# Kernel optimization log

Measured on AMD Instinct MI355X. Metric: run time of the kernel, lower is better.

The kernel has to match this reference:

```python
import jax, jax.numpy as jnp
import numpy as np

N = 10000      # nodes
E = 160000     # edges (before self-loops)
F_IN = 128     # num_features
H1, D1 = 4, 256   # conv1: 4 heads x 256, concat -> 1024
D2 = 256          # conv2: 1 head x 256
NEG_SLOPE = 0.2


def setup_inputs() -> dict:
    key = jax.random.key(0)
    ks = jax.random.split(key, 12)
    def p(k, shape, fan):
        return jax.random.normal(k, shape, jnp.float32) / np.float32(np.sqrt(fan))
    return {
        "x": jax.random.normal(ks[0], (N, F_IN), jnp.float32),
        "edge_index": jax.random.randint(ks[1], (2, E), 0, N, jnp.int32),
        "W1": p(ks[2], (F_IN, H1 * D1), F_IN),
        "att_src1": p(ks[3], (H1, D1), D1),
        "att_dst1": p(ks[4], (H1, D1), D1),
        "b1": jnp.zeros((H1 * D1,), jnp.float32),
        "lin1_W": p(ks[5], (F_IN, H1 * D1), F_IN),
        "lin1_b": jnp.zeros((H1 * D1,), jnp.float32),
        "W2": p(ks[6], (H1 * D1, D2), H1 * D1),
        "att_src2": p(ks[7], (1, D2), D2),
        "att_dst2": p(ks[8], (1, D2), D2),
        "b2": jnp.zeros((D2,), jnp.float32),
        "lin2_W": p(ks[9], (H1 * D1, D2), H1 * D1),
        "lin2_b": jnp.zeros((D2,), jnp.float32),
    }


def gat_layer(x, src, dst, W, a_src, a_dst, b, heads, d):
    """PyG-style GATConv: transform, edgewise LeakyReLU attention,
    segment-softmax over destination neighborhoods, scatter-add, concat heads."""
    n = x.shape[0]
    h = (x @ W).reshape(n, heads, d)                       # [N, H, D]
    s_src = jnp.einsum('nhd,hd->nh', h, a_src)             # per-node scores
    s_dst = jnp.einsum('nhd,hd->nh', h, a_dst)
    e = jax.nn.leaky_relu(s_src[src] + s_dst[dst], NEG_SLOPE)   # [E, H]
    m = jax.ops.segment_max(e, dst, num_segments=n)        # stable softmax per dst
    p = jnp.exp(e - m[dst])
    z = jax.ops.segment_sum(p, dst, num_segments=n)
    alpha = p / (z[dst] + 1e-16)                           # [E, H]
    msg = h[src] * alpha[:, :, None]                       # [E, H, D]
    out = jax.ops.segment_sum(msg, dst, num_segments=n)    # [N, H, D]
    return out.reshape(n, heads * d) + b, alpha


def reference(x, edge_index, W1, att_src1, att_dst1, b1, lin1_W, lin1_b,
              W2, att_src2, att_dst2, b2, lin2_W, lin2_b):
    n = x.shape[0]
    loop = jnp.arange(n, dtype=edge_index.dtype)           # add self-loops (PyG default)
    src = jnp.concatenate([edge_index[0], loop])
    dst = jnp.concatenate([edge_index[1], loop])
    h1, alpha1 = gat_layer(x, src, dst, W1, att_src1, att_dst1, b1, H1, D1)
    h1 = jax.nn.elu(h1 + x @ lin1_W + lin1_b)              # conv1 + lin1 residual, ELU
    h2, _ = gat_layer(h1, src, dst, W2, att_src2, att_dst2, b2, 1, D2)
    out = h2 + h1 @ lin2_W + lin2_b                        # conv2 + lin2 residual
    return out, alpha1
```

## Files before the change

kernel.cpp:

```cpp
#include <hip/hip_runtime.h>
#include <hip/hip_bf16.h>
#include <math.h>

#define NN   10000
#define EE   160000
#define ETOT 170000
#define FIN  128
#define C1   1024
#define NH1  4
#define D1   256
#define D2   256
#define MAXD 96

typedef __attribute__((ext_vector_type(8))) short bf16x8;
typedef __attribute__((ext_vector_type(4))) float f32x4;

__device__ __forceinline__ float b2f(unsigned short u)
{
    union { unsigned int i; float f; } c; c.i = (unsigned int)u << 16; return c.f;
}
__device__ __forceinline__ unsigned short f2b(float x)
{
    return __builtin_bit_cast(unsigned short, __float2bfloat16(x));
}
__device__ __forceinline__ void split1(float x, unsigned short &h, unsigned short &l)
{
    __hip_bfloat16 hb = __float2bfloat16(x);
    float r = x - __bfloat162float(hb);
    h = __builtin_bit_cast(unsigned short, hb);
    l = __builtin_bit_cast(unsigned short, __float2bfloat16(r));
}

__device__ __forceinline__ void split_A_body(const float* __restrict__ X,
                                             unsigned short* __restrict__ A2,
                                             int M, int K, int idx)
{
    int kq4 = K >> 2;
    if (idx >= M * kq4) return;
    int m = idx / kq4, kq = idx % kq4;
    float4 v = *(const float4*)&X[(size_t)m * K + kq * 4];
    ushort4 h, l;
    split1(v.x, h.x, l.x); split1(v.y, h.y, l.y);
    split1(v.z, h.z, l.z); split1(v.w, h.w, l.w);
    unsigned short* row = A2 + (size_t)m * (2 * K);
    *(ushort4*)&row[kq * 4]     = h;
    *(ushort4*)&row[K + kq * 4] = l;
}

__device__ __forceinline__ void split_Bt_body(const float* __restrict__ B0,
                                              const float* __restrict__ B1,
                                              int K, int N0, int Ntot,
                                              unsigned short* __restrict__ Bt, int idx)
{
    int total = Ntot * (K >> 2);
    if (idx >= total) return;
    int n = idx % Ntot;
    int kq = idx / Ntot;
    int k = kq * 4;
    const float* B; int nc, nb;
    if (n < N0) { B = B0; nc = n; nb = N0; }
    else        { B = B1; nc = n - N0; nb = Ntot - N0; }
    float v0 = B[(size_t)(k + 0) * nb + nc];
    float v1 = B[(size_t)(k + 1) * nb + nc];
    float v2 = B[(size_t)(k + 2) * nb + nc];
    float v3 = B[(size_t)(k + 3) * nb + nc];
    ushort4 h, l;
    split1(v0, h.x, l.x); split1(v1, h.y, l.y);
    split1(v2, h.z, l.z); split1(v3, h.w, l.w);
    unsigned short* row = Bt + (size_t)n * (3 * K);
    *(ushort4*)&row[k]         = h;
    *(ushort4*)&row[K + k]     = h;
    *(ushort4*)&row[2 * K + k] = l;
}

__device__ __forceinline__ void split_Bt1_body(const float* __restrict__ W1,
                                               const float* __restrict__ lin1W,
                                               unsigned short* __restrict__ Bt, int idx)
{
    if (idx >= 1024 * 64) return;
    int n = idx & 1023;
    int k = (idx >> 10) * 4;
    float v[4];
    #pragma unroll
    for (int i = 0; i < 4; ++i) {
        int kk = k + i;
        v[i] = (kk < 128) ? W1[(size_t)kk * C1 + n] : lin1W[(size_t)(kk - 128) * C1 + n];
    }
    ushort4 h, l;
    split1(v[0], h.x, l.x); split1(v[1], h.y, l.y);
    split1(v[2], h.z, l.z); split1(v[3], h.w, l.w);
    unsigned short* row = Bt + (size_t)n * 768;
    *(ushort4*)&row[k]       = h;
    *(ushort4*)&row[256 + k] = h;
    *(ushort4*)&row[512 + k] = l;
}

__global__ __launch_bounds__(256)
void prep(const float* __restrict__ x, unsigned short* __restrict__ A1stk,
          const float* __restrict__ W1, const float* __restrict__ lin1_W,
          unsigned short* __restrict__ Bt1,
          const float* __restrict__ W2, const float* __restrict__ lin2_W,
          unsigned short* __restrict__ Bt2,
          const int* __restrict__ dstp, int* __restrict__ cnt,
          const float* __restrict__ as1, const float* __restrict__ ad1,
          float* __restrict__ w1s, float* __restrict__ w1d,
          const float* __restrict__ as2, const float* __restrict__ ad2,
          float* __restrict__ v2s, float* __restrict__ v2d)
{
    const int b = blockIdx.x, t = threadIdx.x;
    const int w = t >> 6, lane = t & 63;
    if (b < 1250) {
        split_A_body(x, A1stk, NN, FIN, b * 256 + t);
    } else if (b < 1506) {
        split_Bt1_body(W1, lin1_W, Bt1, (b - 1250) * 256 + t);
    } else if (b < 2018) {
        split_Bt_body(W2, lin2_W, C1, D2, 512, Bt2, (b - 1506) * 256 + t);
    } else if (b < 2683) {
        int e = (b - 2018) * 256 + t;
        if (e < ETOT) {
            int d = (e < EE) ? dstp[e] : (e - EE);
            atomicAdd(&cnt[d], 1);
        }
    } else if (b < 2939) {
        int gw = (b - 2683) * 4 + w;
        int k = gw >> 3, rem = gw & 7, h = rem >> 1, issd = rem & 1;
        const float* a = issd ? ad1 : as1;
        float4 wv = *(const float4*)&W1[(size_t)k * C1 + h * 256 + lane * 4];
        float4 av = *(const float4*)&a[h * 256 + lane * 4];
        float s = wv.x * av.x + wv.y * av.y + wv.z * av.z + wv.w * av.w;
        #pragma unroll
        for (int off = 32; off; off >>= 1) s += __shfl_xor(s, off);
        if (lane == 0) (issd ? w1d : w1s)[k * 4 + h] = s;
    } else {
        int gw = (b - 2939) * 4 + w;
        int k = gw >> 1, issd = gw & 1;
        const float* a = issd ? ad2 : as2;
        float4 wv = *(const float4*)&W2[(size_t)k * D2 + lane * 4];
        float4 av = *(const float4*)&a[lane * 4];
        float s = wv.x * av.x + wv.y * av.y + wv.z * av.z + wv.w * av.w;
        #pragma unroll
        for (int off = 32; off; off >>= 1) s += __shfl_xor(s, off);
        if (lane == 0) (issd ? v2d : v2s)[k] = s;
    }
}

__device__ __forceinline__ void glds16(const void* g, void* l)
{
    __builtin_amdgcn_global_load_lds((const __attribute__((address_space(1))) void*)g,
                                     (__attribute__((address_space(3))) void*)l, 16, 0, 0);
}

__global__ __launch_bounds__(256)
void gemm_l1(const unsigned short* __restrict__ Apx,
             const unsigned short* __restrict__ Ax,
             const unsigned short* __restrict__ Bt,
             unsigned short* __restrict__ h1split,
             int M, const float* __restrict__ bias0, const float* __restrict__ bias1)
{
    constexpr int BM = 128, BN = 128, BK = 32;
    constexpr int FJ = 4, FI = 4;
    constexpr int SLOTS = 4, SMASK = 3, SWSH = 1;
    constexpr int RPC = 16, ACH = 8, CPW = 4;
    constexpr int ABUF = BM * BK, BBUF = BN * BK;
    __shared__ __align__(16) unsigned short sA[2 * ABUF];
    __shared__ __align__(16) unsigned short sB[2 * BBUF];
    const int tid = threadIdx.x, w = tid >> 6, lane = tid & 63;
    const int cpx = gridDim.x >> 3;
    const int t0 = (blockIdx.x & 7) * cpx + (blockIdx.x >> 3);
    const int m0 = (t0 >> 3) * BM;
    const int n0 = (t0 & 7) * BN;
    const int hsel = n0 >> 8;
    const int wm = w >> 1, wn = w & 1;
    f32x4 acc[FI][FJ] = {};

    const unsigned short *gx[CPW], *gpx[CPW], *gb[CPW];
    int lofs[CPW]; bool isa[CPW];
    {
        const int r = lane / SLOTS, sl = lane % SLOTS;
        const int ssl = sl ^ ((r >> SWSH) & SMASK);
        #pragma unroll
        for (int cc = 0; cc < CPW; ++cc) {
            int c = w * CPW + cc;
            if (c < ACH) {
                int gm = m0 + c * RPC + r; if (gm >= M) gm = M - 1;
                gx[cc]  = Ax  + (size_t)gm * 256 + ssl * 8;
                gpx[cc] = Apx + (size_t)gm * 1024 + hsel * 256 + ssl * 8;
                gb[cc]  = nullptr;
                lofs[cc] = c * 512;
                isa[cc] = true;
            } else {
                int gn = n0 + (c - ACH) * RPC + r;
                gx[cc] = gpx[cc] = nullptr;
                gb[cc] = Bt + (size_t)gn * 768 + ssl * 8;
                lofs[cc] = (c - ACH) * 512;
                isa[cc] = false;
            }
        }
    }

    const int rAl = wm * 64 + (lane & 15);
    const int rBl = wn * 64 + (lane & 15);
    const int sIdx = lane >> 4;
    const int nit = 768 / BK;
    int cur = 0;

    auto stage = [&](int kk, int buf) {
        int rr = kk >> 7;
        bool px = !(rr & 1);
        int off = px ? ((rr == 2) ? 128 : 0) : ((rr == 3) ? 128 : 0);
        int kin = kk & 127;
        #pragma unroll
        for (int cc = 0; cc < CPW; ++cc) {
            if (isa[cc]) glds16((px ? gpx[cc] : gx[cc]) + off + kin, sA + buf * ABUF + lofs[cc]);
            else         glds16(gb[cc] + kk,                         sB + buf * BBUF + lofs[cc]);
        }
    };

    stage(0, 0);
    __syncthreads();
    for (int it = 0; it < nit; ++it) {
        if (it + 1 < nit) stage((it + 1) * BK, cur ^ 1);
        const unsigned short* cA = sA + cur * ABUF;
        const unsigned short* cB = sB + cur * BBUF;
        bf16x8 av[FJ], bv[FI];
        #pragma unroll
        for (int f = 0; f < FI; ++f) {
            int row = rBl + f * 16;
            bv[f] = *(const bf16x8*)&cB[row * BK + ((sIdx ^ ((row >> SWSH) & SMASK)) << 3)];
        }
        #pragma unroll
        for (int f = 0; f < FJ; ++f) {
            int row = rAl + f * 16;
            av[f] = *(const bf16x8*)&cA[row * BK + ((sIdx ^ ((row >> SWSH) & SMASK)) << 3)];
        }
        #pragma unroll
        for (int fj = 0; fj < FJ; ++fj)
            #pragma unroll
            for (int fi = 0; fi < FI; ++fi)
                acc[fi][fj] = __builtin_amdgcn_mfma_f32_16x16x32_bf16(
                    bv[fi], av[fj], acc[fi][fj], 0, 0, 0);
        __syncthreads();
        cur ^= 1;
    }

    const int lrow = lane & 15;
    const int lcol = (lane >> 4) << 2;
    #pragma unroll
    for (int fj = 0; fj < FJ; ++fj) {
        int row = m0 + wm * 64 + fj * 16 + lrow;
        if (row >= M) continue;
        #pragma unroll
        for (int fi = 0; fi < FI; ++fi) {
            int col = n0 + wn * 64 + fi * 16 + lcol;
            f32x4 v = acc[fi][fj];
            const float4 g0 = *(const float4*)&bias0[col];
            const float4 g1 = *(const float4*)&bias1[col];
            v[0] += g0.x + g1.x; v[1] += g0.y + g1.y;
            v[2] += g0.z + g1.z; v[3] += g0.w + g1.w;
            #pragma unroll
            for (int i = 0; i < 4; ++i) v[i] = v[i] > 0.f ? v[i] : expm1f(v[i]);
            ushort4 hi, lo;
            split1(v[0], hi.x, lo.x); split1(v[1], hi.y, lo.y);
            split1(v[2], hi.z, lo.z); split1(v[3], hi.w, lo.w);
            unsigned short* orow = h1split + (size_t)row * 2048;
            *(ushort4*)&orow[col]        = hi;
            *(ushort4*)&orow[C1 + col]   = lo;
        }
    }
}

template<int BN, int WM, int WN, int BK>
__global__ __launch_bounds__(256)
void gemm_split(const unsigned short* __restrict__ A, int lda, int ka2,
                const unsigned short* __restrict__ Bt, int keff,
                unsigned short* __restrict__ outPb, float* __restrict__ outR,
                int M, int nsplit, int ldR, int ntn,
                const float* __restrict__ bias0, const float* __restrict__ bias1)
{
    constexpr int BM   = 128;
    constexpr int WTM  = BM / WM,  WTN = BN / WN;
    constexpr int FJ   = WTM / 16, FI  = WTN / 16;
    constexpr int KS   = BK / 32;
    constexpr int SLOTS = BK / 8;
    constexpr int SMASK = SLOTS - 1;
    constexpr int SWSH  = (BK == 32) ? 1 : 0;
    constexpr int RPC  = 512 / BK;
    constexpr int ACH  = BM / RPC;
    constexpr int NCH  = (BM + BN) / RPC;
    constexpr int CPW  = NCH / 4;
    constexpr int ABUF = BM * BK, BBUF = BN * BK;

    __shared__ __align__(16) unsigned short sA[2 * ABUF];
    __shared__ __align__(16) unsigned short sB[2 * BBUF];

    const int tid = threadIdx.x;
    const int w = tid >> 6, lane = tid & 63;

    const int cpx = gridDim.x >> 3;
    const int t0  = (blockIdx.x & 7) * cpx + (blockIdx.x >> 3);
    const int m0 = (t0 / ntn) * BM;
    const int n0 = (t0 % ntn) * BN;
    const int wm = w / WN, wn = w % WN;

    f32x4 acc[FI][FJ] = {};

    const unsigned short* gp[CPW];
    int lofs[CPW];
    bool isa[CPW];
    {
        const int r  = lane / SLOTS;
        const int sl = lane % SLOTS;
        const int ssl = sl ^ ((r >> SWSH) & SMASK);
        #pragma unroll
        for (int cc = 0; cc < CPW; ++cc) {
            int c = w * CPW + cc;
            if (c < ACH) {
                int gm = m0 + c * RPC + r; if (gm >= M) gm = M - 1;
                gp[cc]   = A + (size_t)gm * lda + ssl * 8;
                lofs[cc] = c * 512;
                isa[cc]  = true;
            } else {
                int gn = n0 + (c - ACH) * RPC + r;
                gp[cc]   = Bt + (size_t)gn * keff + ssl * 8;
                lofs[cc] = (c - ACH) * 512;
                isa[cc]  = false;
            }
        }
    }

    const int rAl = wm * WTM + (lane & 15);
    const int rBl = wn * WTN + (lane & 15);
    const int koff = (lane >> 4) * 8;
    const int nit = keff / BK;
    int cur = 0;

    #pragma unroll
    for (int cc = 0; cc < CPW; ++cc)
        glds16(gp[cc], (isa[cc] ? sA : sB) + lofs[cc]);
    __syncthreads();

    for (int it = 0; it < nit; ++it) {
        if (it + 1 < nit) {
            int kn = (it + 1) * BK;
            int kAn = (kn >= ka2) ? (kn - ka2) : kn;
            #pragma unroll
            for (int cc = 0; cc < CPW; ++cc) {
                unsigned short* dst = (isa[cc] ? sA + (cur ^ 1) * ABUF
                                               : sB + (cur ^ 1) * BBUF) + lofs[cc];
                glds16(gp[cc] + (isa[cc] ? kAn : kn), dst);
            }
        }
        const unsigned short* cA = sA + cur * ABUF;
        const unsigned short* cB = sB + cur * BBUF;
        #pragma unroll
        for (int ks = 0; ks < KS; ++ks) {
            const int sIdx = (ks * 32 + koff) >> 3;
            bf16x8 av[FJ], bv[FI];
            #pragma unroll
            for (int f = 0; f < FI; ++f) {
                int row = rBl + f * 16;
                bv[f] = *(const bf16x8*)&cB[row * BK + ((sIdx ^ ((row >> SWSH) & SMASK)) << 3)];
            }
            #pragma unroll
            for (int f = 0; f < FJ; ++f) {
                int row = rAl + f * 16;
                av[f] = *(const bf16x8*)&cA[row * BK + ((sIdx ^ ((row >> SWSH) & SMASK)) << 3)];
            }
            #pragma unroll
            for (int fj = 0; fj < FJ; ++fj)
                #pragma unroll
                for (int fi = 0; fi < FI; ++fi)
                    acc[fi][fj] = __builtin_amdgcn_mfma_f32_16x16x32_bf16(
                        bv[fi], av[fj], acc[fi][fj], 0, 0, 0);
        }
        __syncthreads();
        cur ^= 1;
    }

    const int lrow = lane & 15;
    const int lcol = (lane >> 4) << 2;
    #pragma unroll
    for (int fj = 0; fj < FJ; ++fj) {
        int row = m0 + wm * WTM + fj * 16 + lrow;
        if (row >= M) continue;
        #pragma unroll
        for (int fi = 0; fi < FI; ++fi) {
            int col = n0 + wn * WTN + fi * 16 + lcol;
            f32x4 v = acc[fi][fj];
            if (col < nsplit) {
                ushort4 o;
                o.x = f2b(v[0]); o.y = f2b(v[1]); o.z = f2b(v[2]); o.w = f2b(v[3]);
                *(ushort4*)&outPb[(size_t)row * nsplit + col] = o;
            } else {
                int c = col - nsplit;
                const float4 g0 = *(const float4*)&bias0[c];
                const float4 g1 = *(const float4*)&bias1[c];
                v[0] += g0.x + g1.x; v[1] += g0.y + g1.y;
                v[2] += g0.z + g1.z; v[3] += g0.w + g1.w;
                *(f32x4*)&outR[(size_t)row * ldR + c] = v;
            }
        }
    }
}

__global__ __launch_bounds__(256)
void s1_scores(const float* __restrict__ x, const float* __restrict__ w1s,
               const float* __restrict__ w1d, float* __restrict__ s_src,
               float* __restrict__ s_dst)
{
    const int n = blockIdx.x * 4 + (threadIdx.x >> 6);
    if (n >= NN) return;
    const int lane = threadIdx.x & 63;
    float2 xv = *(const float2*)&x[(size_t)n * FIN + lane * 2];
    float4 wa = *(const float4*)&w1s[(lane * 2) * 4];
    float4 wb = *(const float4*)&w1s[(lane * 2 + 1) * 4];
    float4 da = *(const float4*)&w1d[(lane * 2) * 4];
    float4 db = *(const float4*)&w1d[(lane * 2 + 1) * 4];
    float ss[4] = { xv.x * wa.x + xv.y * wb.x, xv.x * wa.y + xv.y * wb.y,
                    xv.x * wa.z + xv.y * wb.z, xv.x * wa.w + xv.y * wb.w };
    float sd[4] = { xv.x * da.x + xv.y * db.x, xv.x * da.y + xv.y * db.y,
                    xv.x * da.z + xv.y * db.z, xv.x * da.w + xv.y * db.w };
    #pragma unroll
    for (int off = 32; off; off >>= 1) {
        #pragma unroll
        for (int h = 0; h < 4; ++h) {
            ss[h] += __shfl_xor(ss[h], off);
            sd[h] += __shfl_xor(sd[h], off);
        }
    }
    if (lane == 0) {
        #pragma unroll
        for (int h = 0; h < 4; ++h) {
            s_src[n * NH1 + h] = ss[h];
            s_dst[n * NH1 + h] = sd[h];
        }
    }
}

__global__ __launch_bounds__(256)
void scores2(const unsigned short* __restrict__ h1split, const float* __restrict__ v2s,
             const float* __restrict__ v2d, float* __restrict__ s_src,
             float* __restrict__ s_dst)
{
    const int n = blockIdx.x * 4 + (threadIdx.x >> 6);
    if (n >= NN) return;
    const int lane = threadIdx.x & 63;
    const unsigned short* row = h1split + (size_t)n * 2048 + lane * 16;
    float ss = 0.f, sd = 0.f;
    #pragma unroll
    for (int q = 0; q < 16; ++q) {
        float hv = b2f(row[q]);
        ss += hv * v2s[lane * 16 + q];
        sd += hv * v2d[lane * 16 + q];
    }
    #pragma unroll
    for (int off = 32; off; off >>= 1) {
        ss += __shfl_xor(ss, off);
        sd += __shfl_xor(sd, off);
    }
    if (lane == 0) { s_src[n] = ss; s_dst[n] = sd; }
}

__global__ __launch_bounds__(1024)
void scan_kernel(const int* __restrict__ cnt, int* __restrict__ row_ptr)
{
    __shared__ int part[1024];
    const int t = threadIdx.x;
    int local[10];
    int s = 0;
    #pragma unroll
    for (int j = 0; j < 10; ++j) {
        int idx = t * 10 + j;
        local[j] = s;
        s += (idx < NN) ? cnt[idx] : 0;
    }
    part[t] = s;
    __syncthreads();
    for (int off = 1; off < 1024; off <<= 1) {
        int v = (t >= off) ? part[t - off] : 0;
        __syncthreads();
        part[t] += v;
        __syncthreads();
    }
    int prefix = (t > 0) ? part[t - 1] : 0;
    #pragma unroll
    for (int j = 0; j < 10; ++j) {
        int idx = t * 10 + j;
        if (idx < NN) row_ptr[idx] = prefix + local[j];
    }
    if (t == 0) row_ptr[NN] = ETOT;
}

__global__ void scatter_edges(const int* __restrict__ srcp, const int* __restrict__ dstp,
                              const int* __restrict__ row_ptr, int* __restrict__ fill,
                              int* __restrict__ csr_src, int* __restrict__ csr_eid,
                              int* __restrict__ csr_dst,
                              const float* __restrict__ s_src1,
                              const float* __restrict__ s_dst1,
                              float* __restrict__ sc1)
{
    int e = blockIdx.x * 256 + threadIdx.x;
    if (e >= ETOT) return;
    int s, d;
    if (e < EE) { s = srcp[e]; d = dstp[e]; } else { s = d = e - EE; }
    int pos = row_ptr[d] + atomicAdd(&fill[d], 1);
    csr_src[pos] = s;
    csr_eid[pos] = e;
    csr_dst[pos] = d;
    float4 ss = *(const float4*)&s_src1[s * 4];
    float4 dd = *(const float4*)&s_dst1[d * 4];
    float4 sc;
    sc.x = ss.x + dd.x; sc.y = ss.y + dd.y;
    sc.z = ss.z + dd.z; sc.w = ss.w + dd.w;
    sc.x = sc.x > 0.f ? sc.x : 0.2f * sc.x;
    sc.y = sc.y > 0.f ? sc.y : 0.2f * sc.y;
    sc.z = sc.z > 0.f ? sc.z : 0.2f * sc.z;
    sc.w = sc.w > 0.f ? sc.w : 0.2f * sc.w;
    *(float4*)&sc1[(size_t)pos * 4] = sc;
}

__global__ void sc2_kernel(const int* __restrict__ csr_src, const int* __restrict__ csr_dst,
                           const float* __restrict__ s_src2, const float* __restrict__ s_dst2,
                           float* __restrict__ sc2)
{
    int j = blockIdx.x * 256 + threadIdx.x;
    if (j >= ETOT) return;
    float sc = s_src2[csr_src[j]] + s_dst2[csr_dst[j]];
    sc2[j] = sc > 0.f ? sc : 0.2f * sc;
}

__global__ __launch_bounds__(256)
void px_gather(const float* __restrict__ x, const float* __restrict__ sc1,
               const int* __restrict__ row_ptr,
               const int* __restrict__ csr_src, const int* __restrict__ csr_eid,
               unsigned short* __restrict__ Apx, float* __restrict__ alpha_out)
{
    __shared__ float lalpha[NH1][MAXD];
    __shared__ float lmz[NH1][2];
    __shared__ float red[4][16][33];
    const int n = blockIdx.x;
    const int t = threadIdx.x;
    const int w = t >> 6;
    const int lane = t & 63;
    const int start = row_ptr[n], end = row_ptr[n + 1];

    {
        const int h = w;
        float m = -1e30f;
        for (int i = start + lane; i < end; i += 64)
            m = fmaxf(m, sc1[(size_t)i * 4 + h]);
        #pragma unroll
        for (int off = 32; off; off >>= 1) m = fmaxf(m, __shfl_xor(m, off));
        float z = 0.f;
        for (int i = start + lane; i < end; i += 64)
            z += __expf(sc1[(size_t)i * 4 + h] - m);
        #pragma unroll
        for (int off = 32; off; off >>= 1) z += __shfl_xor(z, off);
        const float invz = 1.f / (z + 1e-16f);
        for (int i = start + lane; i < end; i += 64) {
            float a = __expf(sc1[(size_t)i * 4 + h] - m) * invz;
            alpha_out[(size_t)csr_eid[i] * NH1 + h] = a;
            int idx = i - start;
            if (idx < MAXD) lalpha[h][idx] = a;
        }
        if (lane == 0) { lmz[h][0] = m; lmz[h][1] = invz; }
    }
    __syncthreads();

    const int slot = w * 4 + (lane >> 4);
    const int g = lane & 15;
    float a0, a1, a2, a3;
    float acc[4][8] = {};
    for (int i = start + slot; i < end; i += 16) {
        const int s = csr_src[i];
        const int idx = i - start;
        if (idx < MAXD) {
            a0 = lalpha[0][idx]; a1 = lalpha[1][idx];
            a2 = lalpha[2][idx]; a3 = lalpha[3][idx];
        } else {
            float4 sv = *(const float4*)&sc1[(size_t)i * 4];
            a0 = __expf(sv.x - lmz[0][0]) * lmz[0][1];
            a1 = __expf(sv.y - lmz[1][0]) * lmz[1][1];
            a2 = __expf(sv.z - lmz[2][0]) * lmz[2][1];
            a3 = __expf(sv.w - lmz[3][0]) * lmz[3][1];
        }
        const float* xr = &x[(size_t)s * FIN + g * 8];
        float4 v0 = *(const float4*)&xr[0];
        float4 v1 = *(const float4*)&xr[4];
        float vv[8] = { v0.x, v0.y, v0.z, v0.w, v1.x, v1.y, v1.z, v1.w };
        #pragma unroll
        for (int d = 0; d < 8; ++d) {
            acc[0][d] += a0 * vv[d];
            acc[1][d] += a1 * vv[d];
            acc[2][d] += a2 * vv[d];
            acc[3][d] += a3 * vv[d];
        }
    }
    #pragma unroll
    for (int off = 16; off <= 32; off <<= 1)
        #pragma unroll
        for (int h = 0; h < 4; ++h)
            #pragma unroll
            for (int d = 0; d < 8; ++d)
                acc[h][d] += __shfl_xor(acc[h][d], off);
    if ((lane >> 4) == 0) {
        #pragma unroll
        for (int h = 0; h < 4; ++h)
            #pragma unroll
            for (int d = 0; d < 8; ++d)
                red[w][g][h * 8 + d] = acc[h][d];
    }
    __syncthreads();
    if (lane < 16) {
        float sum[8];
        #pragma unroll
        for (int d = 0; d < 8; ++d)
            sum[d] = red[0][lane][w * 8 + d] + red[1][lane][w * 8 + d]
                   + red[2][lane][w * 8 + d] + red[3][lane][w * 8 + d];
        ushort4 hi0, hi1, lo0, lo1;
        split1(sum[0], hi0.x, lo0.x); split1(sum[1], hi0.y, lo0.y);
        split1(sum[2], hi0.z, lo0.z); split1(sum[3], hi0.w, lo0.w);
        split1(sum[4], hi1.x, lo1.x); split1(sum[5], hi1.y, lo1.y);
        split1(sum[6], hi1.z, lo1.z); split1(sum[7], hi1.w, lo1.w);
        unsigned short* orow = Apx + (size_t)n * 1024 + w * 256 + lane * 8;
        *(ushort4*)&orow[0]       = hi0;
        *(ushort4*)&orow[4]       = hi1;
        *(ushort4*)&orow[128]     = lo0;
        *(ushort4*)&orow[132]     = lo1;
    }
}

__global__ __launch_bounds__(64)
void aggregate2(const unsigned short* __restrict__ h2b, const float* __restrict__ sc2,
                const int* __restrict__ row_ptr, const int* __restrict__ csr_src,
                const float* __restrict__ accin, float* __restrict__ out)
{
    __shared__ float lalpha[MAXD];
    const int n = blockIdx.x;
    const int t = threadIdx.x;
    const int start = row_ptr[n], end = row_ptr[n + 1];

    float m = -1e30f;
    for (int i = start + t; i < end; i += 64) m = fmaxf(m, sc2[i]);
    #pragma unroll
    for (int off = 32; off; off >>= 1) m = fmaxf(m, __shfl_xor(m, off));
    float z = 0.f;
    for (int i = start + t; i < end; i += 64) z += __expf(sc2[i] - m);
    #pragma unroll
    for (int off = 32; off; off >>= 1) z += __shfl_xor(z, off);
    const float invz = 1.f / (z + 1e-16f);
    for (int i = start + t; i < end; i += 64) {
        int idx = i - start;
        if (idx < MAXD) lalpha[idx] = __expf(sc2[i] - m) * invz;
    }
    __syncthreads();

    const int slot = t >> 4, g = t & 15;
    float acc[16] = {};
    for (int i = start + slot; i < end; i += 4) {
        const int idx = i - start;
        float a = (idx < MAXD) ? lalpha[idx] : (__expf(sc2[i] - m) * invz);
        const unsigned short* vr = &h2b[(size_t)csr_src[i] * D2 + g * 16];
        bf16x8 u0 = *(const bf16x8*)&vr[0];
        bf16x8 u1 = *(const bf16x8*)&vr[8];
        #pragma unroll
        for (int d = 0; d < 8; ++d) {
            acc[d]     += a * b2f((unsigned short)u0[d]);
            acc[8 + d] += a * b2f((unsigned short)u1[d]);
        }
    }
    #pragma unroll
    for (int off = 16; off <= 32; off <<= 1)
        #pragma unroll
        for (int d = 0; d < 16; ++d)
            acc[d] += __shfl_xor(acc[d], off);
    if (slot == 0) {
        const float* br = &accin[(size_t)n * D2 + g * 16];
        float* orow = &out[(size_t)n * D2 + g * 16];
        #pragma unroll
        for (int q = 0; q < 4; ++q) {
            float4 b = *(const float4*)&br[q * 4];
            float4 r;
            r.x = acc[q * 4 + 0] + b.x; r.y = acc[q * 4 + 1] + b.y;
            r.z = acc[q * 4 + 2] + b.z; r.w = acc[q * 4 + 3] + b.w;
            *(float4*)&orow[q * 4] = r;
        }
    }
}

extern "C" void kernel_launch(void* const* d_in, const int* in_sizes, int n_in,
                              void* d_out, int out_size, void* d_ws, size_t ws_size,
                              hipStream_t stream)
{
    const float* x        = (const float*)d_in[0];
    const int*   ei       = (const int*)  d_in[1];
    const float* W1       = (const float*)d_in[2];
    const float* att_src1 = (const float*)d_in[3];
    const float* att_dst1 = (const float*)d_in[4];
    const float* b1       = (const float*)d_in[5];
    const float* lin1_W   = (const float*)d_in[6];
    const float* lin1_b   = (const float*)d_in[7];
    const float* W2       = (const float*)d_in[8];
    const float* att_src2 = (const float*)d_in[9];
    const float* att_dst2 = (const float*)d_in[10];
    const float* b2       = (const float*)d_in[11];
    const float* lin2_W   = (const float*)d_in[12];
    const float* lin2_b   = (const float*)d_in[13];
    const int* srcp = ei;
    const int* dstp = ei + EE;

    float* out    = (float*)d_out;
    float* alpha1 = out + (size_t)NN * D2;

    float* fw = (float*)d_ws;
    unsigned short* A1stk = (unsigned short*)fw; fw += (size_t)NN * 256 / 2;
    unsigned short* Apx   = (unsigned short*)fw; fw += (size_t)NN * 1024 / 2;
    unsigned short* A2stk = (unsigned short*)fw; fw += (size_t)NN * 2048 / 2;
    unsigned short* h2b   = (unsigned short*)fw; fw += (size_t)NN * 256 / 2;
    float* acc2   = fw;  fw += (size_t)NN * D2;
    unsigned short* Bt1 = (unsigned short*)fw; fw += (size_t)1024 * 768 / 2;
    unsigned short* Bt2 = (unsigned short*)fw; fw += (size_t)512 * 3072 / 2;
    float* w1s = fw; fw += 512;
    float* w1d = fw; fw += 512;
    float* v2s = fw; fw += 1024;
    float* v2d = fw; fw += 1024;
    float* s_src1 = fw; fw += NN * NH1;
    float* s_dst1 = fw; fw += NN * NH1;
    float* s_src2 = fw; fw += NN;
    float* s_dst2 = fw; fw += NN;
    float* sc1    = fw; fw += (size_t)ETOT * NH1;
    float* sc2    = fw; fw += ETOT;
    int* ip      = (int*)fw;
    int* cnt     = ip;  ip += NN;
    int* fill    = ip;  ip += NN;
    int* row_ptr = ip;  ip += NN + 4;
    int* csr_src = ip;  ip += ETOT;
    int* csr_eid = ip;  ip += ETOT;
    int* csr_dst = ip;  ip += ETOT;

    hipMemsetAsync(cnt, 0, 2 * NN * sizeof(int), stream);

    prep<<<3451, 256, 0, stream>>>(x, A1stk, W1, lin1_W, Bt1, W2, lin2_W, Bt2,
                                   dstp, cnt, att_src1, att_dst1, w1s, w1d,
                                   att_src2, att_dst2, v2s, v2d);

    s1_scores<<<(NN + 3) / 4, 256, 0, stream>>>(x, w1s, w1d, s_src1, s_dst1);

    scan_kernel<<<1, 1024, 0, stream>>>(cnt, row_ptr);
    scatter_edges<<<(ETOT + 255) / 256, 256, 0, stream>>>(srcp, dstp, row_ptr, fill,
                                                          csr_src, csr_eid, csr_dst,
                                                          s_src1, s_dst1, sc1);

    px_gather<<<NN, 256, 0, stream>>>(x, sc1, row_ptr, csr_src, csr_eid, Apx, alpha1);

    gemm_l1<<<79 * 8, 256, 0, stream>>>(Apx, A1stk, Bt1, A2stk, NN, lin1_b, b1);

    scores2<<<(NN + 3) / 4, 256, 0, stream>>>(A2stk, v2s, v2d, s_src2, s_dst2);
    sc2_kernel<<<(ETOT + 255) / 256, 256, 0, stream>>>(csr_src, csr_dst, s_src2, s_dst2, sc2);

    gemm_split<64, 4, 1, 64><<<79 * 8, 256, 0, stream>>>(
        A2stk, 2 * C1, 2 * C1, Bt2, 3 * C1, h2b, acc2, NN, D2, D2, 8, lin2_b, b2);

    aggregate2<<<NN, 64, 0, stream>>>(h2b, sc2, row_ptr, csr_src, acc2, out);
}
```

Baseline: 230.6 us.

## Split segment-softmax stats into separate per-node kernels ahead of gather passes

New measurement: 236.9 us. 2.7% more time.

```diff
diff --git a/kernel.cpp b/kernel.cpp
--- a/kernel.cpp
+++ b/kernel.cpp
@@ -10,7 +10,6 @@
 #define NH1  4
 #define D1   256
 #define D2   256
-#define MAXD 96
 
 typedef __attribute__((ext_vector_type(8))) short bf16x8;
 typedef __attribute__((ext_vector_type(4))) float f32x4;
@@ -530,60 +529,110 @@
 }
 
 __global__ __launch_bounds__(256)
+void mz1_kernel(const float* __restrict__ sc1, const int* __restrict__ row_ptr,
+                float* __restrict__ mz1)
+{
+    const int n = blockIdx.x * 4 + (threadIdx.x >> 6);
+    if (n >= NN) return;
+    const int lane = threadIdx.x & 63;
+    const int start = row_ptr[n], end = row_ptr[n + 1];
+    float4 m = make_float4(-1e30f, -1e30f, -1e30f, -1e30f);
+    for (int i = start + lane; i < end; i += 64) {
+        float4 s = *(const float4*)&sc1[(size_t)i * 4];
+        m.x = fmaxf(m.x, s.x); m.y = fmaxf(m.y, s.y);
+        m.z = fmaxf(m.z, s.z); m.w = fmaxf(m.w, s.w);
+    }
+    #pragma unroll
+    for (int off = 32; off; off >>= 1) {
+        m.x = fmaxf(m.x, __shfl_xor(m.x, off));
+        m.y = fmaxf(m.y, __shfl_xor(m.y, off));
+        m.z = fmaxf(m.z, __shfl_xor(m.z, off));
+        m.w = fmaxf(m.w, __shfl_xor(m.w, off));
+    }
+    float4 z = make_float4(0.f, 0.f, 0.f, 0.f);
+    for (int i = start + lane; i < end; i += 64) {
+        float4 s = *(const float4*)&sc1[(size_t)i * 4];
+        z.x += __expf(s.x - m.x); z.y += __expf(s.y - m.y);
+        z.z += __expf(s.z - m.z); z.w += __expf(s.w - m.w);
+    }
+    #pragma unroll
+    for (int off = 32; off; off >>= 1) {
+        z.x += __shfl_xor(z.x, off); z.y += __shfl_xor(z.y, off);
+        z.z += __shfl_xor(z.z, off); z.w += __shfl_xor(z.w, off);
+    }
+    if (lane == 0) {
+        float4 iz;
+        iz.x = 1.f / (z.x + 1e-16f); iz.y = 1.f / (z.y + 1e-16f);
+        iz.z = 1.f / (z.z + 1e-16f); iz.w = 1.f / (z.w + 1e-16f);
+        *(float4*)&mz1[(size_t)n * 8]     = m;
+        *(float4*)&mz1[(size_t)n * 8 + 4] = iz;
+    }
+}
+
+__global__ void alpha1_kernel(const float* __restrict__ sc1, const int* __restrict__ csr_dst,
+                              const int* __restrict__ csr_eid, const float* __restrict__ mz1,
+                              float* __restrict__ alpha_out)
+{
+    int j = blockIdx.x * 256 + threadIdx.x;
+    if (j >= ETOT) return;
+    float4 s = *(const float4*)&sc1[(size_t)j * 4];
+    int d = csr_dst[j];
+    float4 m  = *(const float4*)&mz1[(size_t)d * 8];
+    float4 iz = *(const float4*)&mz1[(size_t)d * 8 + 4];
+    float4 a;
+    a.x = __expf(s.x - m.x) * iz.x;
+    a.y = __expf(s.y - m.y) * iz.y;
+    a.z = __expf(s.z - m.z) * iz.z;
+    a.w = __expf(s.w - m.w) * iz.w;
+    *(float4*)&alpha_out[(size_t)csr_eid[j] * 4] = a;
+}
+
+__global__ __launch_bounds__(256)
+void mz2_kernel(const float* __restrict__ sc2, const int* __restrict__ row_ptr,
+                float* __restrict__ mz2)
+{
+    const int n = blockIdx.x * 4 + (threadIdx.x >> 6);
+    if (n >= NN) return;
+    const int lane = threadIdx.x & 63;
+    const int start = row_ptr[n], end = row_ptr[n + 1];
+    float m = -1e30f;
+    for (int i = start + lane; i < end; i += 64) m = fmaxf(m, sc2[i]);
+    #pragma unroll
+    for (int off = 32; off; off >>= 1) m = fmaxf(m, __shfl_xor(m, off));
+    float z = 0.f;
+    for (int i = start + lane; i < end; i += 64) z += __expf(sc2[i] - m);
+    #pragma unroll
+    for (int off = 32; off; off >>= 1) z += __shfl_xor(z, off);
+    if (lane == 0) {
+        mz2[(size_t)n * 2]     = m;
+        mz2[(size_t)n * 2 + 1] = 1.f / (z + 1e-16f);
+    }
+}
+
+__global__ __launch_bounds__(256)
 void px_gather(const float* __restrict__ x, const float* __restrict__ sc1,
-               const int* __restrict__ row_ptr,
-               const int* __restrict__ csr_src, const int* __restrict__ csr_eid,
-               unsigned short* __restrict__ Apx, float* __restrict__ alpha_out)
-{
-    __shared__ float lalpha[NH1][MAXD];
-    __shared__ float lmz[NH1][2];
+               const float* __restrict__ mz1, const int* __restrict__ row_ptr,
+               const int* __restrict__ csr_src, unsigned short* __restrict__ Apx)
+{
     __shared__ float red[4][16][33];
     const int n = blockIdx.x;
     const int t = threadIdx.x;
     const int w = t >> 6;
     const int lane = t & 63;
     const int start = row_ptr[n], end = row_ptr[n + 1];
-
-    {
-        const int h = w;
-        float m = -1e30f;
-        for (int i = start + lane; i < end; i += 64)
-            m = fmaxf(m, sc1[(size_t)i * 4 + h]);
-        #pragma unroll
-        for (int off = 32; off; off >>= 1) m = fmaxf(m, __shfl_xor(m, off));
-        float z = 0.f;
-        for (int i = start + lane; i < end; i += 64)
-            z += __expf(sc1[(size_t)i * 4 + h] - m);
-        #pragma unroll
-        for (int off = 32; off; off >>= 1) z += __shfl_xor(z, off);
-        const float invz = 1.f / (z + 1e-16f);
-        for (int i = start + lane; i < end; i += 64) {
-            float a = __expf(sc1[(size_t)i * 4 + h] - m) * invz;
-            alpha_out[(size_t)csr_eid[i] * NH1 + h] = a;
-            int idx = i - start;
-            if (idx < MAXD) lalpha[h][idx] = a;
-        }
-        if (lane == 0) { lmz[h][0] = m; lmz[h][1] = invz; }
-    }
-    __syncthreads();
+    const float4 m  = *(const float4*)&mz1[(size_t)n * 8];
+    const float4 iz = *(const float4*)&mz1[(size_t)n * 8 + 4];
 
     const int slot = w * 4 + (lane >> 4);
     const int g = lane & 15;
-    float a0, a1, a2, a3;
     float acc[4][8] = {};
     for (int i = start + slot; i < end; i += 16) {
         const int s = csr_src[i];
-        const int idx = i - start;
-        if (idx < MAXD) {
-            a0 = lalpha[0][idx]; a1 = lalpha[1][idx];
-            a2 = lalpha[2][idx]; a3 = lalpha[3][idx];
-        } else {
-            float4 sv = *(const float4*)&sc1[(size_t)i * 4];
-            a0 = __expf(sv.x - lmz[0][0]) * lmz[0][1];
-            a1 = __expf(sv.y - lmz[1][0]) * lmz[1][1];
-            a2 = __expf(sv.z - lmz[2][0]) * lmz[2][1];
-            a3 = __expf(sv.w - lmz[3][0]) * lmz[3][1];
-        }
+        float4 sv = *(const float4*)&sc1[(size_t)i * 4];
+        const float a0 = __expf(sv.x - m.x) * iz.x;
+        const float a1 = __expf(sv.y - m.y) * iz.y;
+        const float a2 = __expf(sv.z - m.z) * iz.z;
+        const float a3 = __expf(sv.w - m.w) * iz.w;
         const float* xr = &x[(size_t)s * FIN + g * 8];
         float4 v0 = *(const float4*)&xr[0];
         float4 v1 = *(const float4*)&xr[4];
@@ -632,34 +681,20 @@
 
 __global__ __launch_bounds__(64)
 void aggregate2(const unsigned short* __restrict__ h2b, const float* __restrict__ sc2,
-                const int* __restrict__ row_ptr, const int* __restrict__ csr_src,
-                const float* __restrict__ accin, float* __restrict__ out)
-{
-    __shared__ float lalpha[MAXD];
+                const float* __restrict__ mz2, const int* __restrict__ row_ptr,
+                const int* __restrict__ csr_src, const float* __restrict__ accin,
+                float* __restrict__ out)
+{
     const int n = blockIdx.x;
     const int t = threadIdx.x;
     const int start = row_ptr[n], end = row_ptr[n + 1];
-
-    float m = -1e30f;
-    for (int i = start + t; i < end; i += 64) m = fmaxf(m, sc2[i]);
-    #pragma unroll
-    for (int off = 32; off; off >>= 1) m = fmaxf(m, __shfl_xor(m, off));
-    float z = 0.f;
-    for (int i = start + t; i < end; i += 64) z += __expf(sc2[i] - m);
-    #pragma unroll
-    for (int off = 32; off; off >>= 1) z += __shfl_xor(z, off);
-    const float invz = 1.f / (z + 1e-16f);
-    for (int i = start + t; i < end; i += 64) {
-        int idx = i - start;
-        if (idx < MAXD) lalpha[idx] = __expf(sc2[i] - m) * invz;
-    }
-    __syncthreads();
+    const float m    = mz2[(size_t)n * 2];
+    const float invz = mz2[(size_t)n * 2 + 1];
 
     const int slot = t >> 4, g = t & 15;
     float acc[16] = {};
     for (int i = start + slot; i < end; i += 4) {
-        const int idx = i - start;
-        float a = (idx < MAXD) ? lalpha[idx] : (__expf(sc2[i] - m) * invz);
+        const float a = __expf(sc2[i] - m) * invz;
         const unsigned short* vr = &h2b[(size_t)csr_src[i] * D2 + g * 16];
         bf16x8 u0 = *(const bf16x8*)&vr[0];
         bf16x8 u1 = *(const bf16x8*)&vr[8];
@@ -730,6 +765,8 @@
     float* s_dst2 = fw; fw += NN;
     float* sc1    = fw; fw += (size_t)ETOT * NH1;
     float* sc2    = fw; fw += ETOT;
+    float* mz1    = fw; fw += (size_t)NN * 8;
+    float* mz2    = fw; fw += (size_t)NN * 2;
     int* ip      = (int*)fw;
     int* cnt     = ip;  ip += NN;
     int* fill    = ip;  ip += NN;
@@ -751,15 +788,19 @@
                                                           csr_src, csr_eid, csr_dst,
                                                           s_src1, s_dst1, sc1);
 
-    px_gather<<<NN, 256, 0, stream>>>(x, sc1, row_ptr, csr_src, csr_eid, Apx, alpha1);
+    mz1_kernel<<<(NN + 3) / 4, 256, 0, stream>>>(sc1, row_ptr, mz1);
+    alpha1_kernel<<<(ETOT + 255) / 256, 256, 0, stream>>>(sc1, csr_dst, csr_eid, mz1, alpha1);
+
+    px_gather<<<NN, 256, 0, stream>>>(x, sc1, mz1, row_ptr, csr_src, Apx);
 
     gemm_l1<<<79 * 8, 256, 0, stream>>>(Apx, A1stk, Bt1, A2stk, NN, lin1_b, b1);
 
     scores2<<<(NN + 3) / 4, 256, 0, stream>>>(A2stk, v2s, v2d, s_src2, s_dst2);
     sc2_kernel<<<(ETOT + 255) / 256, 256, 0, stream>>>(csr_src, csr_dst, s_src2, s_dst2, sc2);
+    mz2_kernel<<<(NN + 3) / 4, 256, 0, stream>>>(sc2, row_ptr, mz2);
 
     gemm_split<64, 4, 1, 64><<<79 * 8, 256, 0, stream>>>(
         A2stk, 2 * C1, 2 * C1, Bt2, 3 * C1, h2b, acc2, NN, D2, D2, 8, lin2_b, b2);
 
-    aggregate2<<<NN, 64, 0, stream>>>(h2b, sc2, row_ptr, csr_src, acc2, out);
-}
+    aggregate2<<<NN, 64, 0, stream>>>(h2b, sc2, mz2, row_ptr, csr_src, acc2, out);
+}
```
